# Kernel optimization log

Hardware: AMD Instinct MI355X
Metric: run time of the kernel (lower is better)

Reference implementation:

```python
import jax, jax.numpy as jnp
import numpy as np

D_MODEL, N_HEAD, D_HEAD, N_LAYERS, D_FF = 1024, 16, 64, 6, 4096
SEQ_LEN, MEM_LEN, BATCH, CLAMP_LEN = 512, 128, 4, 512
LN_EPS = 1e-5


def layernorm(x, g, b):
    mu = jnp.mean(x, axis=-1, keepdims=True)
    var = jnp.var(x, axis=-1, keepdims=True)
    return (x - mu) * jax.lax.rsqrt(var + LN_EPS) * g + b


def rel_shift(x):
    # x: (qlen, rlen, B, H) -> Transformer-XL relative shift
    q, r, b, n = x.shape
    zp = jnp.zeros((q, 1, b, n), x.dtype)
    xp = jnp.concatenate([zp, x], axis=1).reshape(r + 1, q, b, n)
    return xp[1:].reshape(q, r, b, n)


def pos_embedding(klen):
    # sinusoidal embedding on positions klen-1 .. 0, clamped at CLAMP_LEN
    pos = jnp.arange(klen - 1, -1, -1.0, dtype=jnp.float32)
    pos = jnp.minimum(pos, float(CLAMP_LEN))
    inv_freq = 1.0 / (10000.0 ** (jnp.arange(0.0, D_MODEL, 2.0) / D_MODEL))
    sin_inp = pos[:, None] * inv_freq[None, :]  # (klen, D/2)
    return jnp.concatenate([jnp.sin(sin_inp), jnp.cos(sin_inp)], axis=-1)  # (klen, D)


def setup_inputs() -> dict:
    key = jax.random.key(0)
    ks = jax.random.split(key, 16)
    s = 0.02
    return {
        "inputs": jax.random.normal(ks[0], (SEQ_LEN, BATCH, D_MODEL), jnp.float32),
        "mems": jax.random.normal(ks[1], (N_LAYERS, MEM_LEN, BATCH, D_MODEL), jnp.float32),
        "r_w_bias": jax.random.normal(ks[2], (N_HEAD, D_HEAD), jnp.float32) * s,
        "r_r_bias": jax.random.normal(ks[3], (N_HEAD, D_HEAD), jnp.float32) * s,
        "qkv_w": jax.random.normal(ks[4], (N_LAYERS, 3 * N_HEAD * D_HEAD, D_MODEL), jnp.float32) * s,
        "r_w": jax.random.normal(ks[5], (N_LAYERS, N_HEAD * D_HEAD, D_MODEL), jnp.float32) * s,
        "o_w": jax.random.normal(ks[6], (N_LAYERS, D_MODEL, N_HEAD * D_HEAD), jnp.float32) * s,
        "ln1_g": jnp.ones((N_LAYERS, D_MODEL), jnp.float32),
        "ln1_b": jnp.zeros((N_LAYERS, D_MODEL), jnp.float32),
        "ff_w1": jax.random.normal(ks[7], (N_LAYERS, D_FF, D_MODEL), jnp.float32) * s,
        "ff_b1": jnp.zeros((N_LAYERS, D_FF), jnp.float32),
        "ff_w2": jax.random.normal(ks[8], (N_LAYERS, D_MODEL, D_FF), jnp.float32) * s,
        "ff_b2": jnp.zeros((N_LAYERS, D_MODEL), jnp.float32),
        "ln2_g": jnp.ones((N_LAYERS, D_MODEL), jnp.float32),
        "ln2_b": jnp.zeros((N_LAYERS, D_MODEL), jnp.float32),
        "fin_g": jnp.ones((D_MODEL,), jnp.float32),
        "fin_b": jnp.zeros((D_MODEL,), jnp.float32),
    }


def reference(inputs, mems, r_w_bias, r_r_bias, qkv_w, r_w, o_w,
              ln1_g, ln1_b, ff_w1, ff_b1, ff_w2, ff_b2, ln2_g, ln2_b,
              fin_g, fin_b):
    qlen, bsz, _ = inputs.shape
    mlen = mems.shape[1]
    klen = mlen + qlen
    scale = 1.0 / np.sqrt(D_HEAD)

    pos_emb = pos_embedding(klen)  # (klen, D)
    # causal mask with memory: True = masked
    attn_mask = jnp.triu(jnp.ones((qlen, klen), bool), k=1 + mlen)

    x = inputs  # (T, B, D)
    for l in range(N_LAYERS):
        # ---- relative multi-head attention (pre_lnorm) ----
        cat = jnp.concatenate([mems[l], x], axis=0)           # (klen, B, D)
        h = layernorm(cat, ln1_g[l], ln1_b[l])
        w_heads = jnp.einsum('kbd,ed->kbe', h, qkv_w[l])      # (klen, B, 3HD)
        r_head_k = jnp.einsum('kd,ed->ke', pos_emb, r_w[l])   # (klen, HD)
        hd = N_HEAD * D_HEAD
        q = w_heads[-qlen:, :, :hd].reshape(qlen, bsz, N_HEAD, D_HEAD)
        k = w_heads[:, :, hd:2 * hd].reshape(klen, bsz, N_HEAD, D_HEAD)
        v = w_heads[:, :, 2 * hd:].reshape(klen, bsz, N_HEAD, D_HEAD)
        r_head_k = r_head_k.reshape(klen, N_HEAD, D_HEAD)

        AC = jnp.einsum('ibnd,jbnd->ijbn', q + r_w_bias, k)
        BD = rel_shift(jnp.einsum('ibnd,jnd->ijbn', q + r_r_bias, r_head_k))
        score = (AC + BD) * scale                              # (q, k, B, H)
        score = jnp.where(attn_mask[:, :, None, None], -jnp.inf, score)
        prob = jax.nn.softmax(score, axis=1)
        attn_vec = jnp.einsum('ijbn,jbnd->ibnd', prob, v).reshape(qlen, bsz, hd)
        attn_out = jnp.einsum('ibe,de->ibd', attn_vec, o_w[l])
        x = x + attn_out

        # ---- position-wise FFN (pre_lnorm) ----
        hf = layernorm(x, ln2_g[l], ln2_b[l])
        hf = jax.nn.relu(jnp.einsum('ibd,fd->ibf', hf, ff_w1[l]) + ff_b1[l])
        hf = jnp.einsum('ibf,df->ibd', hf, ff_w2[l]) + ff_b2[l]
        x = x + hf

    return layernorm(x, fin_g, fin_b)
```

## Files before the change

### kernel.cpp

```cpp
#include <hip/hip_runtime.h>
#include <math.h>
#include <stdint.h>

#define DM    1024
#define NH    16
#define DH    64
#define NL    6
#define DFF   4096
#define QLEN  512
#define MLEN  128
#define B_    4
#define KL    640
#define CLAMP 512
#define EPS   1e-5f

typedef _Float16 f16x8 __attribute__((ext_vector_type(8)));
typedef _Float16 f16x4 __attribute__((ext_vector_type(4)));
typedef float    f32x4 __attribute__((ext_vector_type(4)));

__device__ __forceinline__ void gload16(const void* g, void* l) {
  __builtin_amdgcn_global_load_lds(
      (const __attribute__((address_space(1))) void*)g,
      (__attribute__((address_space(3))) void*)l, 16, 0, 0);
}

__device__ __forceinline__ float block_sum(float v, float* sm4) {
#pragma unroll
  for (int o = 32; o > 0; o >>= 1) v += __shfl_down(v, o, 64);
  int lane = threadIdx.x & 63, wid = threadIdx.x >> 6;
  if (lane == 0) sm4[wid] = v;
  __syncthreads();
  float r = sm4[0] + sm4[1] + sm4[2] + sm4[3];
  __syncthreads();
  return r;
}

__global__ __launch_bounds__(256) void pos_emb_kernel(_Float16* __restrict__ pe) {
  int p = blockIdx.x;
  float pos = fminf((float)(KL - 1 - p), (float)CLAMP);
  for (int f = threadIdx.x; f < 512; f += 256) {
    float inv = powf(10000.0f, -(float)f * (1.0f / 512.0f));
    float a = pos * inv;
    pe[(size_t)p * DM + f]       = (_Float16)sinf(a);
    pe[(size_t)p * DM + 512 + f] = (_Float16)cosf(a);
  }
}

__global__ __launch_bounds__(256) void cast_all_kernel(
    const float* __restrict__ qkv, const float* __restrict__ rw,
    const float* __restrict__ ow, const float* __restrict__ f1,
    const float* __restrict__ f2,
    _Float16* __restrict__ dq, _Float16* __restrict__ dr,
    _Float16* __restrict__ dow, _Float16* __restrict__ d1,
    _Float16* __restrict__ d2) {
  size_t i = (size_t)blockIdx.x * 4096;
  const float* s; _Float16* d; size_t off;
  if (i < 18874368)      { s = qkv; d = dq;  off = 0; }
  else if (i < 25165824) { s = rw;  d = dr;  off = 18874368; }
  else if (i < 31457280) { s = ow;  d = dow; off = 25165824; }
  else if (i < 56623104) { s = f1;  d = d1;  off = 31457280; }
  else                   { s = f2;  d = d2;  off = 56623104; }
  size_t kb = i - off + threadIdx.x * 4;
#pragma unroll
  for (int e = 0; e < 4; ++e) {
    size_t k = kb + e * 1024;
    float4 v = *(const float4*)(s + k);
    f16x4 o = { (_Float16)v.x, (_Float16)v.y, (_Float16)v.z, (_Float16)v.w };
    *(f16x4*)(d + k) = o;
  }
}

template <int OUTF16>
__global__ __launch_bounds__(256) void ln_kernel(
    const float* __restrict__ src0, const float* __restrict__ src1,
    const float* __restrict__ g, const float* __restrict__ b,
    float* __restrict__ outf, _Float16* __restrict__ outh, int rows0) {
  __shared__ float sm4[4];
  int row = blockIdx.x;
  const float* src = (row < rows0) ? (src0 + (size_t)row * DM)
                                   : (src1 + (size_t)(row - rows0) * DM);
  float4 v = ((const float4*)src)[threadIdx.x];
  float mean = block_sum(v.x + v.y + v.z + v.w, sm4) * (1.0f / DM);
  float dx = v.x - mean, dy = v.y - mean, dz = v.z - mean, dw = v.w - mean;
  float var = block_sum(dx * dx + dy * dy + dz * dz + dw * dw, sm4) * (1.0f / DM);
  float rstd = rsqrtf(var + EPS);
  float4 gg = ((const float4*)g)[threadIdx.x];
  float4 bb = ((const float4*)b)[threadIdx.x];
  float ox = dx * rstd * gg.x + bb.x;
  float oy = dy * rstd * gg.y + bb.y;
  float oz = dz * rstd * gg.z + bb.z;
  float ow = dw * rstd * gg.w + bb.w;
  if (OUTF16) {
    f16x4 o = { (_Float16)ox, (_Float16)oy, (_Float16)oz, (_Float16)ow };
    *(f16x4*)(outh + (size_t)row * DM + threadIdx.x * 4) = o;
  } else {
    float4 o = { ox, oy, oz, ow };
    ((float4*)(outf + (size_t)row * DM))[threadIdx.x] = o;
  }
}

template <int SK, int BIAS, int OUTF16>
__global__ __launch_bounds__(256) void reduce_ln_kernel(
    const _Float16* __restrict__ pk, const float* __restrict__ bias,
    const float* __restrict__ resid, const float* __restrict__ g,
    const float* __restrict__ b, float* __restrict__ xout,
    _Float16* __restrict__ houth, float* __restrict__ houtf, int MN) {
  __shared__ float sm4[4];
  const int row = blockIdx.x;
  const int c = threadIdx.x * 4;
  const size_t base = (size_t)row * DM + c;
  float s[4] = {};
#pragma unroll
  for (int z = 0; z < SK; ++z) {
    f16x4 v = *(const f16x4*)(pk + (size_t)z * MN + base);
#pragma unroll
    for (int e = 0; e < 4; ++e) s[e] += (float)v[e];
  }
  if (BIAS) {
    float4 bv = *(const float4*)(bias + c);
    s[0] += bv.x; s[1] += bv.y; s[2] += bv.z; s[3] += bv.w;
  }
  float4 rv = *(const float4*)(resid + base);
  s[0] += rv.x; s[1] += rv.y; s[2] += rv.z; s[3] += rv.w;
  float4 xo = { s[0], s[1], s[2], s[3] };
  *(float4*)(xout + base) = xo;
  float mean = block_sum(s[0] + s[1] + s[2] + s[3], sm4) * (1.0f / DM);
  float d0 = s[0] - mean, d1 = s[1] - mean, d2 = s[2] - mean, d3 = s[3] - mean;
  float var = block_sum(d0 * d0 + d1 * d1 + d2 * d2 + d3 * d3, sm4) * (1.0f / DM);
  float rstd = rsqrtf(var + EPS);
  float4 gg = *(const float4*)(g + c);
  float4 bb = *(const float4*)(b + c);
  float o0 = d0 * rstd * gg.x + bb.x, o1 = d1 * rstd * gg.y + bb.y;
  float o2 = d2 * rstd * gg.z + bb.z, o3 = d3 * rstd * gg.w + bb.w;
  if (OUTF16) {
    f16x4 oh = { (_Float16)o0, (_Float16)o1, (_Float16)o2, (_Float16)o3 };
    *(f16x4*)(houth + base) = oh;
  } else {
    float4 of = { o0, o1, o2, o3 };
    *(float4*)(houtf + base) = of;
  }
}

template <int BIAS, int RELU, int RESID, int OUTF16>
__global__ __launch_bounds__(256) void gemm_mfma(
    const _Float16* __restrict__ A, const _Float16* __restrict__ B,
    const float* __restrict__ bias, const float* __restrict__ resid,
    float* __restrict__ Cf, _Float16* __restrict__ Ch,
    int M, int N, int K) {
  __shared__ alignas(16) _Float16 As[128 * 32];
  __shared__ alignas(16) _Float16 Bs[128 * 32];
  const int t = threadIdx.x;
  const int lane = t & 63, wid = t >> 6;
  const int m0 = blockIdx.y * 128, n0 = blockIdx.x * 128;
  const int wm = (wid >> 1) * 64, wn = (wid & 1) * 64;

  const int c0 = wid * 64 + lane, c1 = c0 + 256;
  const _Float16* Ap0 = A + (size_t)(m0 + (c0 >> 2)) * K + (c0 & 3) * 8;
  const _Float16* Ap1 = A + (size_t)(m0 + (c1 >> 2)) * K + (c1 & 3) * 8;
  const _Float16* Bp0 = B + (size_t)(n0 + (c0 >> 2)) * K + (c0 & 3) * 8;
  const _Float16* Bp1 = B + (size_t)(n0 + (c1 >> 2)) * K + (c1 & 3) * 8;
  _Float16* Asw0 = &As[wid * 512];
  _Float16* Asw1 = &As[wid * 512 + 2048];
  _Float16* Bsw0 = &Bs[wid * 512];
  _Float16* Bsw1 = &Bs[wid * 512 + 2048];

  f32x4 acc[4][4] = {};
  for (int k0 = 0; k0 < K; k0 += 32) {
    __syncthreads();
    gload16(Ap0 + k0, Asw0);
    gload16(Ap1 + k0, Asw1);
    gload16(Bp0 + k0, Bsw0);
    gload16(Bp1 + k0, Bsw1);
    __syncthreads();
    f16x8 af[4], bf[4];
#pragma unroll
    for (int f = 0; f < 4; ++f) {
      af[f] = *(const f16x8*)&As[(wm + f * 16 + (lane & 15)) * 32 + (lane >> 4) * 8];
      bf[f] = *(const f16x8*)&Bs[(wn + f * 16 + (lane & 15)) * 32 + (lane >> 4) * 8];
    }
#pragma unroll
    for (int i = 0; i < 4; ++i)
#pragma unroll
      for (int j = 0; j < 4; ++j)
        acc[i][j] = __builtin_amdgcn_mfma_f32_16x16x32_f16(af[i], bf[j], acc[i][j], 0, 0, 0);
  }
#pragma unroll
  for (int i = 0; i < 4; ++i) {
#pragma unroll
    for (int j = 0; j < 4; ++j) {
      const int n = n0 + wn + j * 16 + (lane & 15);
      float bv = 0.0f;
      if (BIAS) bv = bias[n];
#pragma unroll
      for (int r = 0; r < 4; ++r) {
        const int m = m0 + wm + i * 16 + (lane >> 4) * 4 + r;
        float v = acc[i][j][r] + bv;
        if (RELU) v = fmaxf(v, 0.0f);
        if (RESID) v += resid[(size_t)m * N + n];
        if (OUTF16) Ch[(size_t)m * N + n] = (_Float16)v;
        else        Cf[(size_t)m * N + n] = v;
      }
    }
  }
}

__global__ __launch_bounds__(256) void gemm_sk(
    const _Float16* __restrict__ A, const _Float16* __restrict__ B,
    _Float16* __restrict__ pk, int M, int N, int K, int Ks) {
  __shared__ alignas(16) _Float16 As[128 * 32];
  __shared__ alignas(16) _Float16 Bs[128 * 32];
  const int t = threadIdx.x;
  const int lane = t & 63, wid = t >> 6;
  const int m0 = blockIdx.y * 128, n0 = blockIdx.x * 128;
  const int z = blockIdx.z;
  const int kbase = z * Ks;
  const int wm = (wid >> 1) * 64, wn = (wid & 1) * 64;

  const int c0 = wid * 64 + lane, c1 = c0 + 256;
  const _Float16* Ap0 = A + (size_t)(m0 + (c0 >> 2)) * K + kbase + (c0 & 3) * 8;
  const _Float16* Ap1 = A + (size_t)(m0 + (c1 >> 2)) * K + kbase + (c1 & 3) * 8;
  const _Float16* Bp0 = B + (size_t)(n0 + (c0 >> 2)) * K + kbase + (c0 & 3) * 8;
  const _Float16* Bp1 = B + (size_t)(n0 + (c1 >> 2)) * K + kbase + (c1 & 3) * 8;
  _Float16* Asw0 = &As[wid * 512];
  _Float16* Asw1 = &As[wid * 512 + 2048];
  _Float16* Bsw0 = &Bs[wid * 512];
  _Float16* Bsw1 = &Bs[wid * 512 + 2048];

  f32x4 acc[4][4] = {};
  for (int k0 = 0; k0 < Ks; k0 += 32) {
    __syncthreads();
    gload16(Ap0 + k0, Asw0);
    gload16(Ap1 + k0, Asw1);
    gload16(Bp0 + k0, Bsw0);
    gload16(Bp1 + k0, Bsw1);
    __syncthreads();
    f16x8 af[4], bf[4];
#pragma unroll
    for (int f = 0; f < 4; ++f) {
      af[f] = *(const f16x8*)&As[(wm + f * 16 + (lane & 15)) * 32 + (lane >> 4) * 8];
      bf[f] = *(const f16x8*)&Bs[(wn + f * 16 + (lane & 15)) * 32 + (lane >> 4) * 8];
    }
#pragma unroll
    for (int i = 0; i < 4; ++i)
#pragma unroll
      for (int j = 0; j < 4; ++j)
        acc[i][j] = __builtin_amdgcn_mfma_f32_16x16x32_f16(af[i], bf[j], acc[i][j], 0, 0, 0);
  }
  _Float16* out = pk + (size_t)z * M * N;
#pragma unroll
  for (int i = 0; i < 4; ++i)
#pragma unroll
    for (int j = 0; j < 4; ++j) {
      const int n = n0 + wn + j * 16 + (lane & 15);
#pragma unroll
      for (int r = 0; r < 4; ++r) {
        const int m = m0 + wm + i * 16 + (lane >> 4) * 4 + r;
        out[(size_t)m * N + n] = (_Float16)acc[i][j][r];
      }
    }
}

template <int SK, int OUTF16>
__global__ __launch_bounds__(256) void reduce_k(
    const _Float16* __restrict__ pk, float* __restrict__ Cf,
    _Float16* __restrict__ Ch, int MN) {
  const int idx = (blockIdx.x * 256 + threadIdx.x) * 8;
  float s[8] = {};
#pragma unroll
  for (int zz = 0; zz < SK; ++zz) {
    f16x8 v = *(const f16x8*)(pk + (size_t)zz * MN + idx);
#pragma unroll
    for (int e = 0; e < 8; ++e) s[e] += (float)v[e];
  }
  if (OUTF16) {
    f16x8 o;
#pragma unroll
    for (int e = 0; e < 8; ++e) o[e] = (_Float16)s[e];
    *(f16x8*)(Ch + idx) = o;
  } else {
    float4 o0 = { s[0], s[1], s[2], s[3] };
    float4 o1 = { s[4], s[5], s[6], s[7] };
    *(float4*)(Cf + idx) = o0;
    *(float4*)(Cf + idx + 4) = o1;
  }
}

__global__ __launch_bounds__(256, 3) void attn_kernel(
    const _Float16* __restrict__ wh,
    const _Float16* __restrict__ rk,
    const float* __restrict__ rwb,
    const float* __restrict__ rrb,
    _Float16* __restrict__ po,
    float* __restrict__ pm,
    float* __restrict__ pl) {
  __shared__ alignas(16) _Float16 KS[64 * 72];
  __shared__ alignas(16) _Float16 VT[64 * 72];
  __shared__ alignas(16) _Float16 RR[128 * 72];
  __shared__ alignas(16) _Float16 QS[4][16 * 72];

  const int i0 = blockIdx.x * 64, n = blockIdx.y;
  const int b = blockIdx.z & 3, zz = blockIdx.z >> 2;
  const int t = threadIdx.x, lane = t & 63, wid = t >> 6;
  const int g = lane >> 4, li = lane & 15;
  const int strip = wid * 16;
  _Float16* QSw = QS[wid];

  f16x8 qw[2], qr[2];
#pragma unroll
  for (int ks_ = 0; ks_ < 2; ++ks_) {
    const _Float16* qp =
        wh + ((size_t)(MLEN + i0 + strip + li) * B_ + b) * 3072 + n * 64 + ks_ * 32 + g * 8;
    f16x8 qv = *(const f16x8*)qp;
#pragma unroll
    for (int e = 0; e < 8; ++e) {
      float f0 = (float)qv[e];
      qw[ks_][e] = (_Float16)(f0 + rwb[n * 64 + ks_ * 32 + g * 8 + e]);
      qr[ks_][e] = (_Float16)(f0 + rrb[n * 64 + ks_ * 32 + g * 8 + e]);
    }
  }

  f32x4 o_[4] = {};
  float mrun[4], lrun[4];
#pragma unroll
  for (int r = 0; r < 4; ++r) { mrun[r] = -INFINITY; lrun[r] = 0.0f; }

  const float SC = 0.125f * 1.44269504f;
  const int ntiles = i0 / 64 + 3;
  for (int tt = zz; tt < ntiles; tt += 4) {
    const int j0 = tt * 64;
    __syncthreads();
    {
      int row = t >> 2, c = (t & 3) * 16;
      const _Float16* kp = wh + ((size_t)(j0 + row) * B_ + b) * 3072 + 1024 + n * 64 + c;
      *(f16x8*)&KS[row * 72 + c] = *(const f16x8*)kp;
      *(f16x8*)&KS[row * 72 + c + 8] = *(const f16x8*)(kp + 8);
    }
#pragma unroll
    for (int it = 0; it < 2; ++it) {
      int j = t & 63, d0 = (t >> 6) * 8 + it * 32;
      f16x8 vv = *(const f16x8*)(wh + ((size_t)(j0 + j) * B_ + b) * 3072 + 2048 + n * 64 + d0);
#pragma unroll
      for (int e = 0; e < 8; ++e) VT[(d0 + e) * 72 + j] = vv[e];
    }
    {
      int row = t >> 1, c = (t & 1) * 32;
      int mrow = j0 - i0 + 448 + row;
      if (mrow > KL - 1) mrow = KL - 1;
      const _Float16* rp = rk + (size_t)mrow * 6144 + n * 64 + c;
#pragma unroll
      for (int cc = 0; cc < 32; cc += 8)
        *(f16x8*)&RR[row * 72 + c + cc] = *(const f16x8*)(rp + cc);
    }
    __syncthreads();
    f32x4 acs[4] = {};
#pragma unroll
    for (int ks_ = 0; ks_ < 2; ++ks_)
#pragma unroll
      for (int cf = 0; cf < 4; ++cf) {
        f16x8 bk = *(const f16x8*)&KS[(cf * 16 + li) * 72 + ks_ * 32 + g * 8];
        acs[cf] = __builtin_amdgcn_mfma_f32_16x16x32_f16(qw[ks_], bk, acs[cf], 0, 0, 0);
      }
#pragma unroll
    for (int half = 0; half < 2; ++half) {
      f32x4 acq[4] = {};
#pragma unroll
      for (int ks_ = 0; ks_ < 2; ++ks_)
#pragma unroll
        for (int cf = 0; cf < 4; ++cf) {
          f16x8 br = *(const f16x8*)&RR[((half * 4 + cf) * 16 + li) * 72 + ks_ * 32 + g * 8];
          acq[cf] = __builtin_amdgcn_mfma_f32_16x16x32_f16(qr[ks_], br, acq[cf], 0, 0, 0);
        }
#pragma unroll
      for (int cf = 0; cf < 4; ++cf)
#pragma unroll
        for (int r = 0; r < 4; ++r) {
          int il = strip + g * 4 + r;
          int jl = (half * 4 + cf) * 16 + li - 63 + il;
          if ((unsigned)jl < 64u) QSw[(g * 4 + r) * 72 + jl] = (_Float16)acq[cf][r];
        }
    }
    float pf[4][4], fac[4];
#pragma unroll
    for (int r = 0; r < 4; ++r) {
      int il = strip + g * 4 + r, gi = i0 + il;
      float sv[4], mx = -INFINITY;
#pragma unroll
      for (int cf = 0; cf < 4; ++cf) {
        int jl = cf * 16 + li;
        float v = (acs[cf][r] + (float)QSw[(g * 4 + r) * 72 + jl]) * SC;
        if (j0 + jl > gi + MLEN) v = -INFINITY;
        sv[cf] = v;
        mx = fmaxf(mx, v);
      }
#pragma unroll
      for (int o2 = 1; o2 < 16; o2 <<= 1) mx = fmaxf(mx, __shfl_xor(mx, o2, 64));
      float mnew = fmaxf(mrun[r], mx);
      float fc = exp2f(mrun[r] - mnew);
      float sum = 0.0f;
#pragma unroll
      for (int cf = 0; cf < 4; ++cf) { pf[cf][r] = exp2f(sv[cf] - mnew); sum += pf[cf][r]; }
#pragma unroll
      for (int o2 = 1; o2 < 16; o2 <<= 1) sum += __shfl_xor(sum, o2, 64);
      lrun[r] = lrun[r] * fc + sum;
      mrun[r] = mnew;
      fac[r] = fc;
    }
#pragma unroll
    for (int cf = 0; cf < 4; ++cf)
#pragma unroll
      for (int r = 0; r < 4; ++r)
        QSw[(g * 4 + r) * 72 + cf * 16 + li] = (_Float16)pf[cf][r];
#pragma unroll
    for (int cf = 0; cf < 4; ++cf)
#pragma unroll
      for (int r = 0; r < 4; ++r)
        o_[cf][r] *= fac[r];
#pragma unroll
    for (int ks_ = 0; ks_ < 2; ++ks_) {
      f16x8 pa = *(const f16x8*)&QSw[li * 72 + ks_ * 32 + g * 8];
#pragma unroll
      for (int cf = 0; cf < 4; ++cf) {
        f16x8 bv = *(const f16x8*)&VT[(cf * 16 + li) * 72 + ks_ * 32 + g * 8];
        o_[cf] = __builtin_amdgcn_mfma_f32_16x16x32_f16(pa, bv, o_[cf], 0, 0, 0);
      }
    }
  }
  const size_t obase = (size_t)zz * (QLEN * B_ * 1024);
#pragma unroll
  for (int cf = 0; cf < 4; ++cf)
#pragma unroll
    for (int r = 0; r < 4; ++r) {
      int row = strip + g * 4 + r;
      float l = lrun[r];
      float oo = (l > 0.0f) ? o_[cf][r] / l : 0.0f;
      po[obase + ((size_t)(i0 + row) * B_ + b) * 1024 + n * 64 + cf * 16 + li] = (_Float16)oo;
    }
  if (li == 0) {
#pragma unroll
    for (int r = 0; r < 4; ++r) {
      int row = strip + g * 4 + r;
      int idx = ((i0 + row) * B_ + b) * 16 + n;
      pm[zz * 32768 + idx] = (lrun[r] > 0.0f) ? mrun[r] : -3.0e38f;
      pl[zz * 32768 + idx] = lrun[r];
    }
  }
}

__global__ __launch_bounds__(256) void attn_combine(
    const _Float16* __restrict__ po, const float* __restrict__ pm,
    const float* __restrict__ pl, _Float16* __restrict__ av) {
  const size_t e = ((size_t)blockIdx.x * 256 + threadIdx.x) * 8;
  const int mlidx = (int)(e >> 10) * 16 + (((int)e & 1023) >> 6);
  float m[4], l[4];
#pragma unroll
  for (int z = 0; z < 4; ++z) { m[z] = pm[z * 32768 + mlidx]; l[z] = pl[z * 32768 + mlidx]; }
  float M = fmaxf(fmaxf(m[0], m[1]), fmaxf(m[2], m[3]));
  float w[4], wsum = 0.0f;
#pragma unroll
  for (int z = 0; z < 4; ++z) { w[z] = l[z] * exp2f(m[z] - M); wsum += w[z]; }
  float inv = 1.0f / wsum;
  float s[8] = {};
#pragma unroll
  for (int z = 0; z < 4; ++z) {
    f16x8 oz = *(const f16x8*)(po + (size_t)z * 2097152 + e);
    float wz = w[z] * inv;
#pragma unroll
    for (int k = 0; k < 8; ++k) s[k] += wz * (float)oz[k];
  }
  f16x8 o;
#pragma unroll
  for (int k = 0; k < 8; ++k) o[k] = (_Float16)s[k];
  *(f16x8*)(av + e) = o;
}

extern "C" void kernel_launch(void* const* d_in, const int* in_sizes, int n_in,
                              void* d_out, int out_size, void* d_ws, size_t ws_size,
                              hipStream_t stream) {
  const float* inputs = (const float*)d_in[0];
  const float* mems   = (const float*)d_in[1];
  const float* rwb    = (const float*)d_in[2];
  const float* rrb    = (const float*)d_in[3];
  const float* qkv_w  = (const float*)d_in[4];
  const float* r_w    = (const float*)d_in[5];
  const float* o_w    = (const float*)d_in[6];
  const float* ln1_g  = (const float*)d_in[7];
  const float* ln1_b  = (const float*)d_in[8];
  const float* ff_w1  = (const float*)d_in[9];
  const float* ff_b1  = (const float*)d_in[10];
  const float* ff_w2  = (const float*)d_in[11];
  const float* ff_b2  = (const float*)d_in[12];
  const float* ln2_g  = (const float*)d_in[13];
  const float* ln2_b  = (const float*)d_in[14];
  const float* fin_g  = (const float*)d_in[15];
  const float* fin_b  = (const float*)d_in[16];
  float* out = (float*)d_out;

  float* ws = (float*)d_ws;
  float* xbuf = ws;
  _Float16* fb = (_Float16*)(ws + 2097152);
  _Float16* wh_h   = fb;
  _Float16* rk_all = wh_h + 7864320;
  _Float16* pe_h   = rk_all + 3932160;
  _Float16* h_h    = pe_h + 655360;
  _Float16* av_h   = h_h + 2621440;
  _Float16* ffh_h  = av_h + 2097152;
  _Float16* pk     = ffh_h + 8388608;
  _Float16* po     = pk + 8388608;
  float*    pm     = (float*)(po + 8388608);
  float*    pl     = pm + 131072;
  _Float16* wq_all = (_Float16*)(pl + 131072);
  _Float16* rw_all = wq_all + 18874368;
  _Float16* wo_all = rw_all + 6291456;
  _Float16* w1_all = wo_all + 6291456;
  _Float16* w2_all = w1_all + 25165824;

  pos_emb_kernel<<<KL, 256, 0, stream>>>(pe_h);
  cast_all_kernel<<<19968, 256, 0, stream>>>(
      qkv_w, r_w, o_w, ff_w1, ff_w2, wq_all, rw_all, wo_all, w1_all, w2_all);
  gemm_sk<<<dim3(6144 / 128, 640 / 128, 2), 256, 0, stream>>>(
      pe_h, rw_all, pk, KL, 6144, DM, DM / 2);
  reduce_k<2, 1><<<KL * 6144 / 2048, 256, 0, stream>>>(
      pk, nullptr, rk_all, KL * 6144);

  ln_kernel<1><<<KL * B_, 256, 0, stream>>>(
      mems, inputs, ln1_g, ln1_b, nullptr, h_h, MLEN * B_);

  const float* xcur = inputs;
  for (int l = 0; l < NL; ++l) {
    gemm_mfma<0, 0, 0, 1><<<dim3(3072 / 128, 2560 / 128), 256, 0, stream>>>(
        h_h, wq_all + (size_t)l * 3145728, nullptr, nullptr, nullptr, wh_h, 2560, 3072, DM);
    attn_kernel<<<dim3(QLEN / 64, NH, B_ * 4), 256, 0, stream>>>(
        wh_h, rk_all + (size_t)l * 1024, rwb, rrb, po, pm, pl);
    attn_combine<<<1024, 256, 0, stream>>>(po, pm, pl, av_h);
    gemm_sk<<<dim3(DM / 128, (QLEN * B_) / 128, 4), 256, 0, stream>>>(
        av_h, wo_all + (size_t)l * 1048576, pk, QLEN * B_, DM, DM, DM / 4);
    reduce_ln_kernel<4, 0, 1><<<QLEN * B_, 256, 0, stream>>>(
        pk, nullptr, xcur, ln2_g + l * DM, ln2_b + l * DM, xbuf, h_h, nullptr,
        QLEN * B_ * DM);
    gemm_mfma<1, 1, 0, 1><<<dim3(DFF / 128, (QLEN * B_) / 128), 256, 0, stream>>>(
        h_h, w1_all + (size_t)l * 4194304, ff_b1 + (size_t)l * DFF, nullptr,
        nullptr, ffh_h, QLEN * B_, DFF, DM);
    gemm_sk<<<dim3(DM / 128, (QLEN * B_) / 128, 4), 256, 0, stream>>>(
        ffh_h, w2_all + (size_t)l * 4194304, pk, QLEN * B_, DM, DFF, DFF / 4);
    if (l < NL - 1) {
      reduce_ln_kernel<4, 1, 1><<<QLEN * B_, 256, 0, stream>>>(
          pk, ff_b2 + (size_t)l * DM, xbuf, ln1_g + (size_t)(l + 1) * DM,
          ln1_b + (size_t)(l + 1) * DM, xbuf, h_h + 524288, nullptr,
          QLEN * B_ * DM);
      ln_kernel<1><<<MLEN * B_, 256, 0, stream>>>(
          mems + (size_t)(l + 1) * MLEN * B_ * DM, nullptr,
          ln1_g + (size_t)(l + 1) * DM, ln1_b + (size_t)(l + 1) * DM,
          nullptr, h_h, 1 << 30);
    } else {
      reduce_ln_kernel<4, 1, 0><<<QLEN * B_, 256, 0, stream>>>(
          pk, ff_b2 + (size_t)l * DM, xbuf, fin_g, fin_b, xbuf, nullptr, out,
          QLEN * B_ * DM);
    }
    xcur = xbuf;
  }
}
```

Measured before the change: 1.213 ms.

## Fuse fp32-to-fp16 weight cast into GEMM tile loads, drop cast kernel

```diff
diff --git a/kernel.cpp b/kernel.cpp
--- a/kernel.cpp
+++ b/kernel.cpp
@@ -43,30 +43,6 @@
     float a = pos * inv;
     pe[(size_t)p * DM + f]       = (_Float16)sinf(a);
     pe[(size_t)p * DM + 512 + f] = (_Float16)cosf(a);
-  }
-}
-
-__global__ __launch_bounds__(256) void cast_all_kernel(
-    const float* __restrict__ qkv, const float* __restrict__ rw,
-    const float* __restrict__ ow, const float* __restrict__ f1,
-    const float* __restrict__ f2,
-    _Float16* __restrict__ dq, _Float16* __restrict__ dr,
-    _Float16* __restrict__ dow, _Float16* __restrict__ d1,
-    _Float16* __restrict__ d2) {
-  size_t i = (size_t)blockIdx.x * 4096;
-  const float* s; _Float16* d; size_t off;
-  if (i < 18874368)      { s = qkv; d = dq;  off = 0; }
-  else if (i < 25165824) { s = rw;  d = dr;  off = 18874368; }
-  else if (i < 31457280) { s = ow;  d = dow; off = 25165824; }
-  else if (i < 56623104) { s = f1;  d = d1;  off = 31457280; }
-  else                   { s = f2;  d = d2;  off = 56623104; }
-  size_t kb = i - off + threadIdx.x * 4;
-#pragma unroll
-  for (int e = 0; e < 4; ++e) {
-    size_t k = kb + e * 1024;
-    float4 v = *(const float4*)(s + k);
-    f16x4 o = { (_Float16)v.x, (_Float16)v.y, (_Float16)v.z, (_Float16)v.w };
-    *(f16x4*)(d + k) = o;
   }
 }
 
@@ -143,40 +119,54 @@
 
 template <int BIAS, int RELU, int RESID, int OUTF16>
 __global__ __launch_bounds__(256) void gemm_mfma(
-    const _Float16* __restrict__ A, const _Float16* __restrict__ B,
+    const _Float16* __restrict__ A, const float* __restrict__ B,
     const float* __restrict__ bias, const float* __restrict__ resid,
     float* __restrict__ Cf, _Float16* __restrict__ Ch,
     int M, int N, int K) {
   __shared__ alignas(16) _Float16 As[128 * 32];
-  __shared__ alignas(16) _Float16 Bs[128 * 32];
+  __shared__ alignas(16) float Bs[128 * 32];
   const int t = threadIdx.x;
   const int lane = t & 63, wid = t >> 6;
+  const int li = lane & 15, g = lane >> 4;
   const int m0 = blockIdx.y * 128, n0 = blockIdx.x * 128;
   const int wm = (wid >> 1) * 64, wn = (wid & 1) * 64;
 
   const int c0 = wid * 64 + lane, c1 = c0 + 256;
   const _Float16* Ap0 = A + (size_t)(m0 + (c0 >> 2)) * K + (c0 & 3) * 8;
   const _Float16* Ap1 = A + (size_t)(m0 + (c1 >> 2)) * K + (c1 & 3) * 8;
-  const _Float16* Bp0 = B + (size_t)(n0 + (c0 >> 2)) * K + (c0 & 3) * 8;
-  const _Float16* Bp1 = B + (size_t)(n0 + (c1 >> 2)) * K + (c1 & 3) * 8;
   _Float16* Asw0 = &As[wid * 512];
   _Float16* Asw1 = &As[wid * 512 + 2048];
-  _Float16* Bsw0 = &Bs[wid * 512];
-  _Float16* Bsw1 = &Bs[wid * 512 + 2048];
+  const float* Bp[4];
+  float* Bsw[4];
+#pragma unroll
+  for (int it = 0; it < 4; ++it) {
+    int cb = it * 256 + wid * 64 + lane;
+    int rr = cb >> 3, ss = cb & 7;
+    Bp[it] = B + (size_t)(n0 + rr) * K + (ss ^ (rr & 7)) * 4;
+    Bsw[it] = &Bs[(it * 256 + wid * 64) * 4];
+  }
+  const int sa = ((2 * g) ^ (li & 7)) * 4;
+  const int sb = ((2 * g + 1) ^ (li & 7)) * 4;
 
   f32x4 acc[4][4] = {};
   for (int k0 = 0; k0 < K; k0 += 32) {
     __syncthreads();
     gload16(Ap0 + k0, Asw0);
     gload16(Ap1 + k0, Asw1);
-    gload16(Bp0 + k0, Bsw0);
-    gload16(Bp1 + k0, Bsw1);
+#pragma unroll
+    for (int it = 0; it < 4; ++it) gload16(Bp[it] + k0, Bsw[it]);
     __syncthreads();
     f16x8 af[4], bf[4];
 #pragma unroll
     for (int f = 0; f < 4; ++f) {
-      af[f] = *(const f16x8*)&As[(wm + f * 16 + (lane & 15)) * 32 + (lane >> 4) * 8];
-      bf[f] = *(const f16x8*)&Bs[(wn + f * 16 + (lane & 15)) * 32 + (lane >> 4) * 8];
+      af[f] = *(const f16x8*)&As[(wm + f * 16 + li) * 32 + g * 8];
+      const float* bpr = &Bs[(wn + f * 16 + li) * 32];
+      f32x4 b0 = *(const f32x4*)(bpr + sa);
+      f32x4 b1 = *(const f32x4*)(bpr + sb);
+      f16x8 h;
+#pragma unroll
+      for (int e = 0; e < 4; ++e) { h[e] = (_Float16)b0[e]; h[e + 4] = (_Float16)b1[e]; }
+      bf[f] = h;
     }
 #pragma unroll
     for (int i = 0; i < 4; ++i)
@@ -188,12 +178,12 @@
   for (int i = 0; i < 4; ++i) {
 #pragma unroll
     for (int j = 0; j < 4; ++j) {
-      const int n = n0 + wn + j * 16 + (lane & 15);
+      const int n = n0 + wn + j * 16 + li;
       float bv = 0.0f;
       if (BIAS) bv = bias[n];
 #pragma unroll
       for (int r = 0; r < 4; ++r) {
-        const int m = m0 + wm + i * 16 + (lane >> 4) * 4 + r;
+        const int m = m0 + wm + i * 16 + g * 4 + r;
         float v = acc[i][j][r] + bv;
         if (RELU) v = fmaxf(v, 0.0f);
         if (RESID) v += resid[(size_t)m * N + n];
@@ -205,12 +195,13 @@
 }
 
 __global__ __launch_bounds__(256) void gemm_sk(
-    const _Float16* __restrict__ A, const _Float16* __restrict__ B,
+    const _Float16* __restrict__ A, const float* __restrict__ B,
     _Float16* __restrict__ pk, int M, int N, int K, int Ks) {
   __shared__ alignas(16) _Float16 As[128 * 32];
-  __shared__ alignas(16) _Float16 Bs[128 * 32];
+  __shared__ alignas(16) float Bs[128 * 32];
   const int t = threadIdx.x;
   const int lane = t & 63, wid = t >> 6;
+  const int li = lane & 15, g = lane >> 4;
   const int m0 = blockIdx.y * 128, n0 = blockIdx.x * 128;
   const int z = blockIdx.z;
   const int kbase = z * Ks;
@@ -219,26 +210,39 @@
   const int c0 = wid * 64 + lane, c1 = c0 + 256;
   const _Float16* Ap0 = A + (size_t)(m0 + (c0 >> 2)) * K + kbase + (c0 & 3) * 8;
   const _Float16* Ap1 = A + (size_t)(m0 + (c1 >> 2)) * K + kbase + (c1 & 3) * 8;
-  const _Float16* Bp0 = B + (size_t)(n0 + (c0 >> 2)) * K + kbase + (c0 & 3) * 8;
-  const _Float16* Bp1 = B + (size_t)(n0 + (c1 >> 2)) * K + kbase + (c1 & 3) * 8;
   _Float16* Asw0 = &As[wid * 512];
   _Float16* Asw1 = &As[wid * 512 + 2048];
-  _Float16* Bsw0 = &Bs[wid * 512];
-  _Float16* Bsw1 = &Bs[wid * 512 + 2048];
+  const float* Bp[4];
+  float* Bsw[4];
+#pragma unroll
+  for (int it = 0; it < 4; ++it) {
+    int cb = it * 256 + wid * 64 + lane;
+    int rr = cb >> 3, ss = cb & 7;
+    Bp[it] = B + (size_t)(n0 + rr) * K + kbase + (ss ^ (rr & 7)) * 4;
+    Bsw[it] = &Bs[(it * 256 + wid * 64) * 4];
+  }
+  const int sa = ((2 * g) ^ (li & 7)) * 4;
+  const int sb = ((2 * g + 1) ^ (li & 7)) * 4;
 
   f32x4 acc[4][4] = {};
   for (int k0 = 0; k0 < Ks; k0 += 32) {
     __syncthreads();
     gload16(Ap0 + k0, Asw0);
     gload16(Ap1 + k0, Asw1);
-    gload16(Bp0 + k0, Bsw0);
-    gload16(Bp1 + k0, Bsw1);
+#pragma unroll
+    for (int it = 0; it < 4; ++it) gload16(Bp[it] + k0, Bsw[it]);
     __syncthreads();
     f16x8 af[4], bf[4];
 #pragma unroll
     for (int f = 0; f < 4; ++f) {
-      af[f] = *(const f16x8*)&As[(wm + f * 16 + (lane & 15)) * 32 + (lane >> 4) * 8];
-      bf[f] = *(const f16x8*)&Bs[(wn + f * 16 + (lane & 15)) * 32 + (lane >> 4) * 8];
+      af[f] = *(const f16x8*)&As[(wm + f * 16 + li) * 32 + g * 8];
+      const float* bpr = &Bs[(wn + f * 16 + li) * 32];
+      f32x4 b0 = *(const f32x4*)(bpr + sa);
+      f32x4 b1 = *(const f32x4*)(bpr + sb);
+      f16x8 h;
+#pragma unroll
+      for (int e = 0; e < 4; ++e) { h[e] = (_Float16)b0[e]; h[e + 4] = (_Float16)b1[e]; }
+      bf[f] = h;
     }
 #pragma unroll
     for (int i = 0; i < 4; ++i)
@@ -251,10 +255,10 @@
   for (int i = 0; i < 4; ++i)
 #pragma unroll
     for (int j = 0; j < 4; ++j) {
-      const int n = n0 + wn + j * 16 + (lane & 15);
+      const int n = n0 + wn + j * 16 + li;
 #pragma unroll
       for (int r = 0; r < 4; ++r) {
-        const int m = m0 + wm + i * 16 + (lane >> 4) * 4 + r;
+        const int m = m0 + wm + i * 16 + g * 4 + r;
         out[(size_t)m * N + n] = (_Float16)acc[i][j][r];
       }
     }
@@ -508,17 +512,10 @@
   _Float16* po     = pk + 8388608;
   float*    pm     = (float*)(po + 8388608);
   float*    pl     = pm + 131072;
-  _Float16* wq_all = (_Float16*)(pl + 131072);
-  _Float16* rw_all = wq_all + 18874368;
-  _Float16* wo_all = rw_all + 6291456;
-  _Float16* w1_all = wo_all + 6291456;
-  _Float16* w2_all = w1_all + 25165824;
 
   pos_emb_kernel<<<KL, 256, 0, stream>>>(pe_h);
-  cast_all_kernel<<<19968, 256, 0, stream>>>(
-      qkv_w, r_w, o_w, ff_w1, ff_w2, wq_all, rw_all, wo_all, w1_all, w2_all);
   gemm_sk<<<dim3(6144 / 128, 640 / 128, 2), 256, 0, stream>>>(
-      pe_h, rw_all, pk, KL, 6144, DM, DM / 2);
+      pe_h, r_w, pk, KL, 6144, DM, DM / 2);
   reduce_k<2, 1><<<KL * 6144 / 2048, 256, 0, stream>>>(
       pk, nullptr, rk_all, KL * 6144);
 
@@ -528,20 +525,20 @@
   const float* xcur = inputs;
   for (int l = 0; l < NL; ++l) {
     gemm_mfma<0, 0, 0, 1><<<dim3(3072 / 128, 2560 / 128), 256, 0, stream>>>(
-        h_h, wq_all + (size_t)l * 3145728, nullptr, nullptr, nullptr, wh_h, 2560, 3072, DM);
+        h_h, qkv_w + (size_t)l * 3145728, nullptr, nullptr, nullptr, wh_h, 2560, 3072, DM);
     attn_kernel<<<dim3(QLEN / 64, NH, B_ * 4), 256, 0, stream>>>(
         wh_h, rk_all + (size_t)l * 1024, rwb, rrb, po, pm, pl);
     attn_combine<<<1024, 256, 0, stream>>>(po, pm, pl, av_h);
     gemm_sk<<<dim3(DM / 128, (QLEN * B_) / 128, 4), 256, 0, stream>>>(
-        av_h, wo_all + (size_t)l * 1048576, pk, QLEN * B_, DM, DM, DM / 4);
+        av_h, o_w + (size_t)l * 1048576, pk, QLEN * B_, DM, DM, DM / 4);
     reduce_ln_kernel<4, 0, 1><<<QLEN * B_, 256, 0, stream>>>(
         pk, nullptr, xcur, ln2_g + l * DM, ln2_b + l * DM, xbuf, h_h, nullptr,
         QLEN * B_ * DM);
     gemm_mfma<1, 1, 0, 1><<<dim3(DFF / 128, (QLEN * B_) / 128), 256, 0, stream>>>(
-        h_h, w1_all + (size_t)l * 4194304, ff_b1 + (size_t)l * DFF, nullptr,
+        h_h, ff_w1 + (size_t)l * 4194304, ff_b1 + (size_t)l * DFF, nullptr,
         nullptr, ffh_h, QLEN * B_, DFF, DM);
     gemm_sk<<<dim3(DM / 128, (QLEN * B_) / 128, 4), 256, 0, stream>>>(
-        ffh_h, w2_all + (size_t)l * 4194304, pk, QLEN * B_, DM, DFF, DFF / 4);
+        ffh_h, ff_w2 + (size_t)l * 4194304, pk, QLEN * B_, DM, DFF, DFF / 4);
     if (l < NL - 1) {
       reduce_ln_kernel<4, 1, 1><<<QLEN * B_, 256, 0, stream>>>(
           pk, ff_b2 + (size_t)l * DM, xbuf, ln1_g + (size_t)(l + 1) * DM,
```

New measurement: 1.340 ms. +10.5%, slower.

## Double GEMM K-tile to 64 with XOR-swizzled LDS layout

Applied to the files above, without the earlier changes.

```diff
diff --git a/kernel.cpp b/kernel.cpp
--- a/kernel.cpp
+++ b/kernel.cpp
@@ -147,53 +147,61 @@
     const float* __restrict__ bias, const float* __restrict__ resid,
     float* __restrict__ Cf, _Float16* __restrict__ Ch,
     int M, int N, int K) {
-  __shared__ alignas(16) _Float16 As[128 * 32];
-  __shared__ alignas(16) _Float16 Bs[128 * 32];
+  __shared__ alignas(16) _Float16 As[128 * 64];
+  __shared__ alignas(16) _Float16 Bs[128 * 64];
   const int t = threadIdx.x;
   const int lane = t & 63, wid = t >> 6;
+  const int li = lane & 15, g = lane >> 4;
   const int m0 = blockIdx.y * 128, n0 = blockIdx.x * 128;
   const int wm = (wid >> 1) * 64, wn = (wid & 1) * 64;
 
-  const int c0 = wid * 64 + lane, c1 = c0 + 256;
-  const _Float16* Ap0 = A + (size_t)(m0 + (c0 >> 2)) * K + (c0 & 3) * 8;
-  const _Float16* Ap1 = A + (size_t)(m0 + (c1 >> 2)) * K + (c1 & 3) * 8;
-  const _Float16* Bp0 = B + (size_t)(n0 + (c0 >> 2)) * K + (c0 & 3) * 8;
-  const _Float16* Bp1 = B + (size_t)(n0 + (c1 >> 2)) * K + (c1 & 3) * 8;
-  _Float16* Asw0 = &As[wid * 512];
-  _Float16* Asw1 = &As[wid * 512 + 2048];
-  _Float16* Bsw0 = &Bs[wid * 512];
-  _Float16* Bsw1 = &Bs[wid * 512 + 2048];
+  const _Float16* Ap[4];
+  const _Float16* Bp[4];
+  _Float16 *Asw[4], *Bsw[4];
+#pragma unroll
+  for (int it = 0; it < 4; ++it) {
+    int c = it * 256 + wid * 64 + lane;
+    int rr = c >> 3, gk = ((c & 7) ^ (rr & 7)) * 8;
+    Ap[it] = A + (size_t)(m0 + rr) * K + gk;
+    Bp[it] = B + (size_t)(n0 + rr) * K + gk;
+    Asw[it] = &As[(it * 256 + wid * 64) * 8];
+    Bsw[it] = &Bs[(it * 256 + wid * 64) * 8];
+  }
 
   f32x4 acc[4][4] = {};
-  for (int k0 = 0; k0 < K; k0 += 32) {
+  for (int k0 = 0; k0 < K; k0 += 64) {
     __syncthreads();
-    gload16(Ap0 + k0, Asw0);
-    gload16(Ap1 + k0, Asw1);
-    gload16(Bp0 + k0, Bsw0);
-    gload16(Bp1 + k0, Bsw1);
+#pragma unroll
+    for (int it = 0; it < 4; ++it) gload16(Ap[it] + k0, Asw[it]);
+#pragma unroll
+    for (int it = 0; it < 4; ++it) gload16(Bp[it] + k0, Bsw[it]);
     __syncthreads();
-    f16x8 af[4], bf[4];
-#pragma unroll
-    for (int f = 0; f < 4; ++f) {
-      af[f] = *(const f16x8*)&As[(wm + f * 16 + (lane & 15)) * 32 + (lane >> 4) * 8];
-      bf[f] = *(const f16x8*)&Bs[(wn + f * 16 + (lane & 15)) * 32 + (lane >> 4) * 8];
-    }
-#pragma unroll
-    for (int i = 0; i < 4; ++i)
-#pragma unroll
-      for (int j = 0; j < 4; ++j)
-        acc[i][j] = __builtin_amdgcn_mfma_f32_16x16x32_f16(af[i], bf[j], acc[i][j], 0, 0, 0);
+#pragma unroll
+    for (int kh = 0; kh < 2; ++kh) {
+      f16x8 af[4], bf[4];
+      const int sl = ((kh * 4 + g) ^ (li & 7)) * 8;
+#pragma unroll
+      for (int f = 0; f < 4; ++f) {
+        af[f] = *(const f16x8*)&As[(wm + f * 16 + li) * 64 + sl];
+        bf[f] = *(const f16x8*)&Bs[(wn + f * 16 + li) * 64 + sl];
+      }
+#pragma unroll
+      for (int i = 0; i < 4; ++i)
+#pragma unroll
+        for (int j = 0; j < 4; ++j)
+          acc[i][j] = __builtin_amdgcn_mfma_f32_16x16x32_f16(af[i], bf[j], acc[i][j], 0, 0, 0);
+    }
   }
 #pragma unroll
   for (int i = 0; i < 4; ++i) {
 #pragma unroll
     for (int j = 0; j < 4; ++j) {
-      const int n = n0 + wn + j * 16 + (lane & 15);
+      const int n = n0 + wn + j * 16 + li;
       float bv = 0.0f;
       if (BIAS) bv = bias[n];
 #pragma unroll
       for (int r = 0; r < 4; ++r) {
-        const int m = m0 + wm + i * 16 + (lane >> 4) * 4 + r;
+        const int m = m0 + wm + i * 16 + g * 4 + r;
         float v = acc[i][j][r] + bv;
         if (RELU) v = fmaxf(v, 0.0f);
         if (RESID) v += resid[(size_t)m * N + n];
@@ -207,54 +215,62 @@
 __global__ __launch_bounds__(256) void gemm_sk(
     const _Float16* __restrict__ A, const _Float16* __restrict__ B,
     _Float16* __restrict__ pk, int M, int N, int K, int Ks) {
-  __shared__ alignas(16) _Float16 As[128 * 32];
-  __shared__ alignas(16) _Float16 Bs[128 * 32];
+  __shared__ alignas(16) _Float16 As[128 * 64];
+  __shared__ alignas(16) _Float16 Bs[128 * 64];
   const int t = threadIdx.x;
   const int lane = t & 63, wid = t >> 6;
+  const int li = lane & 15, g = lane >> 4;
   const int m0 = blockIdx.y * 128, n0 = blockIdx.x * 128;
   const int z = blockIdx.z;
   const int kbase = z * Ks;
   const int wm = (wid >> 1) * 64, wn = (wid & 1) * 64;
 
-  const int c0 = wid * 64 + lane, c1 = c0 + 256;
-  const _Float16* Ap0 = A + (size_t)(m0 + (c0 >> 2)) * K + kbase + (c0 & 3) * 8;
-  const _Float16* Ap1 = A + (size_t)(m0 + (c1 >> 2)) * K + kbase + (c1 & 3) * 8;
-  const _Float16* Bp0 = B + (size_t)(n0 + (c0 >> 2)) * K + kbase + (c0 & 3) * 8;
-  const _Float16* Bp1 = B + (size_t)(n0 + (c1 >> 2)) * K + kbase + (c1 & 3) * 8;
-  _Float16* Asw0 = &As[wid * 512];
-  _Float16* Asw1 = &As[wid * 512 + 2048];
-  _Float16* Bsw0 = &Bs[wid * 512];
-  _Float16* Bsw1 = &Bs[wid * 512 + 2048];
+  const _Float16* Ap[4];
+  const _Float16* Bp[4];
+  _Float16 *Asw[4], *Bsw[4];
+#pragma unroll
+  for (int it = 0; it < 4; ++it) {
+    int c = it * 256 + wid * 64 + lane;
+    int rr = c >> 3, gk = ((c & 7) ^ (rr & 7)) * 8;
+    Ap[it] = A + (size_t)(m0 + rr) * K + kbase + gk;
+    Bp[it] = B + (size_t)(n0 + rr) * K + kbase + gk;
+    Asw[it] = &As[(it * 256 + wid * 64) * 8];
+    Bsw[it] = &Bs[(it * 256 + wid * 64) * 8];
+  }
 
   f32x4 acc[4][4] = {};
-  for (int k0 = 0; k0 < Ks; k0 += 32) {
+  for (int k0 = 0; k0 < Ks; k0 += 64) {
     __syncthreads();
-    gload16(Ap0 + k0, Asw0);
-    gload16(Ap1 + k0, Asw1);
-    gload16(Bp0 + k0, Bsw0);
-    gload16(Bp1 + k0, Bsw1);
+#pragma unroll
+    for (int it = 0; it < 4; ++it) gload16(Ap[it] + k0, Asw[it]);
+#pragma unroll
+    for (int it = 0; it < 4; ++it) gload16(Bp[it] + k0, Bsw[it]);
     __syncthreads();
-    f16x8 af[4], bf[4];
-#pragma unroll
-    for (int f = 0; f < 4; ++f) {
-      af[f] = *(const f16x8*)&As[(wm + f * 16 + (lane & 15)) * 32 + (lane >> 4) * 8];
-      bf[f] = *(const f16x8*)&Bs[(wn + f * 16 + (lane & 15)) * 32 + (lane >> 4) * 8];
-    }
-#pragma unroll
-    for (int i = 0; i < 4; ++i)
-#pragma unroll
-      for (int j = 0; j < 4; ++j)
-        acc[i][j] = __builtin_amdgcn_mfma_f32_16x16x32_f16(af[i], bf[j], acc[i][j], 0, 0, 0);
+#pragma unroll
+    for (int kh = 0; kh < 2; ++kh) {
+      f16x8 af[4], bf[4];
+      const int sl = ((kh * 4 + g) ^ (li & 7)) * 8;
+#pragma unroll
+      for (int f = 0; f < 4; ++f) {
+        af[f] = *(const f16x8*)&As[(wm + f * 16 + li) * 64 + sl];
+        bf[f] = *(const f16x8*)&Bs[(wn + f * 16 + li) * 64 + sl];
+      }
+#pragma unroll
+      for (int i = 0; i < 4; ++i)
+#pragma unroll
+        for (int j = 0; j < 4; ++j)
+          acc[i][j] = __builtin_amdgcn_mfma_f32_16x16x32_f16(af[i], bf[j], acc[i][j], 0, 0, 0);
+    }
   }
   _Float16* out = pk + (size_t)z * M * N;
 #pragma unroll
   for (int i = 0; i < 4; ++i)
 #pragma unroll
     for (int j = 0; j < 4; ++j) {
-      const int n = n0 + wn + j * 16 + (lane & 15);
+      const int n = n0 + wn + j * 16 + li;
 #pragma unroll
       for (int r = 0; r < 4; ++r) {
-        const int m = m0 + wm + i * 16 + (lane >> 4) * 4 + r;
+        const int m = m0 + wm + i * 16 + g * 4 + r;
         out[(size_t)m * N + n] = (_Float16)acc[i][j][r];
       }
     }
```

Result: faster. 1.108 ms (-8.6%).
